# Kernel optimization log

Measured on AMD Instinct MI355X. Metric: run time of the kernel, lower is better.

Reference implementation:

```python
import jax, jax.numpy as jnp
import numpy as np

N_QUBITS = 4
N_LAYERS = 2
BN_EPS = 1e-5


def setup_inputs() -> dict:
    key = jax.random.key(0)
    k1, k2 = jax.random.split(key, 2)
    x = jax.random.normal(k1, (131072, 1, 28, 28), dtype=jnp.float32)
    q_params = jax.random.normal(k2, (N_LAYERS, N_QUBITS, 2), dtype=jnp.float32)
    gamma = jnp.ones((N_QUBITS,), dtype=jnp.float32)   # BatchNorm1d weight (init 1)
    beta = jnp.zeros((N_QUBITS,), dtype=jnp.float32)   # BatchNorm1d bias  (init 0)
    return {"x": x, "q_params": q_params, "gamma": gamma, "beta": beta}


def _apply_1q(state, U, w):
    """Apply 2x2 unitary U (shared across batch) on wire w. state: [B,2,2,2,2]."""
    s = jnp.moveaxis(state, 1 + w, -1)
    s = jnp.einsum('...j,ij->...i', s, U)
    return jnp.moveaxis(s, -1, 1 + w)


def _cnot(state, c, t):
    """CNOT with control c, target t on batched statevector [B,2,2,2,2]."""
    s = jnp.moveaxis(state, (1 + c, 1 + t), (-2, -1))
    s = jnp.stack([s[..., 0, :], s[..., 1, ::-1]], axis=-2)
    return jnp.moveaxis(s, (-2, -1), (1 + c, 1 + t))


def _circuit(enc, q_params):
    """Batched analytic statevector sim. enc: [B,4] RX angles -> [B,4] <Z_i>."""
    half = 0.5 * enc
    # RX(theta)|0> = [cos(t/2), -i sin(t/2)]; initial state is the outer product
    q = jnp.stack([jnp.cos(half).astype(jnp.complex64),
                   (-1j) * jnp.sin(half).astype(jnp.complex64)], axis=-1)  # [B,4,2]
    state = jnp.einsum('bi,bj,bk,bl->bijkl', q[:, 0], q[:, 1], q[:, 2], q[:, 3])
    for l in range(N_LAYERS):
        # RZ layer: pure diagonal phase, fuse all 4 wires into one [2,2,2,2] phase tensor
        a = 0.5 * q_params[l, :, 0]
        p = jnp.stack([jnp.exp(-1j * a), jnp.exp(1j * a)], axis=-1)  # [4,2]
        phase = jnp.einsum('i,j,k,l->ijkl', p[0], p[1], p[2], p[3])
        state = state * phase[None]
        # CNOT chain
        for c in range(N_QUBITS - 1):
            state = _cnot(state, c, c + 1)
        # RY layer
        b = 0.5 * q_params[l, :, 1]
        cb, sb = jnp.cos(b), jnp.sin(b)
        for w in range(N_QUBITS):
            U = jnp.stack([jnp.stack([cb[w], -sb[w]]),
                           jnp.stack([sb[w], cb[w]])]).astype(jnp.complex64)
            state = _apply_1q(state, U, w)
    probs = state.real ** 2 + state.imag ** 2  # [B,2,2,2,2]
    zs = []
    sign = jnp.array([1.0, -1.0], dtype=jnp.float32)
    for w in range(N_QUBITS):
        shp = [1] * 5
        shp[1 + w] = 2
        zs.append(jnp.sum(probs * sign.reshape(shp), axis=(1, 2, 3, 4)))
    return jnp.stack(zs, axis=1)  # [B,4]


def reference(x, q_params, gamma, beta):
    bsz = x.shape[0]
    # avg_pool2d(x, 6): kernel=stride=6, VALID -> [B,1,4,4]
    pooled = jax.lax.reduce_window(x, 0.0, jax.lax.add,
                                   (1, 1, 6, 6), (1, 1, 6, 6), 'VALID') / 36.0
    enc = pooled.reshape(bsz, -1)[:, :N_QUBITS]  # [B,4]
    out = _circuit(enc, q_params)                # [B,4]
    # BatchNorm1d in training mode: batch stats, biased variance
    mean = jnp.mean(out, axis=0)
    var = jnp.mean((out - mean) ** 2, axis=0)
    return (out - mean) / jnp.sqrt(var + BN_EPS) * gamma + beta
```

## Files before the change

### kernel.cpp

```cpp
#include <hip/hip_runtime.h>


__global__ __launch_bounds__(256) void qfc_main(
    const float* __restrict__ x,
    const float* __restrict__ qp,
    float* __restrict__ out,
    float* __restrict__ partials)
{
    const int tid  = threadIdx.x;
    const int gt   = blockIdx.x * 256 + tid;
    const int b    = gt >> 1;
    const int half = gt & 1;
    const float* px = x + (size_t)b * 784 + half * (3 * 28);

    float enc[4] = {0.f, 0.f, 0.f, 0.f};
    #pragma unroll
    for (int r = 0; r < 3; ++r) {
        const float4* row = (const float4*)(px + r * 28);
        #pragma unroll
        for (int q = 0; q < 6; ++q) {
            float4 v = row[q];
            const int c0 = q * 4;
            enc[(c0 + 0) / 6] += v.x;
            enc[(c0 + 1) / 6] += v.y;
            enc[(c0 + 2) / 6] += v.z;
            enc[(c0 + 3) / 6] += v.w;
        }
    }
    #pragma unroll
    for (int j = 0; j < 4; ++j)
        enc[j] += __shfl_xor(enc[j], 1, 64);

    float ch[4], sh[4];
    #pragma unroll
    for (int w = 0; w < 4; ++w) {
        float h = enc[w] * (0.5f / 36.0f);
        __sincosf(h, &sh[w], &ch[w]);
    }

    float sr[16], si[16];
    #pragma unroll
    for (int idx = 0; idx < 16; ++idx) {
        float m = 1.f; int k = 0;
        #pragma unroll
        for (int w = 0; w < 4; ++w) {
            if ((idx >> (3 - w)) & 1) { m *= sh[w]; ++k; }
            else                        m *= ch[w];
        }
        switch (k & 3) {
            case 0:  sr[idx] =  m;  si[idx] = 0.f; break;
            case 1:  sr[idx] = 0.f; si[idx] = -m;  break;
            case 2:  sr[idx] = -m;  si[idx] = 0.f; break;
            default: sr[idx] = 0.f; si[idx] =  m;  break;
        }
    }

    #pragma unroll
    for (int l = 0; l < 2; ++l) {
        #pragma unroll
        for (int w = 0; w < 4; ++w) {
            float a = 0.5f * qp[l * 8 + w * 2 + 0];
            float sa, ca; __sincosf(a, &sa, &ca);
            #pragma unroll
            for (int idx = 0; idx < 16; ++idx) {
                float sg = ((idx >> (3 - w)) & 1) ? sa : -sa;
                float r = sr[idx], mm = si[idx];
                sr[idx] = r * ca - mm * sg;
                si[idx] = r * sg + mm * ca;
            }
        }
        #pragma unroll
        for (int c = 0; c < 3; ++c) {
            const int t = c + 1;
            #pragma unroll
            for (int idx = 0; idx < 16; ++idx) {
                if ((((idx >> (3 - c)) & 1) == 1) && (((idx >> (3 - t)) & 1) == 0)) {
                    const int j = idx | (1 << (3 - t));
                    float tr = sr[idx]; sr[idx] = sr[j]; sr[j] = tr;
                    float ti = si[idx]; si[idx] = si[j]; si[j] = ti;
                }
            }
        }
        #pragma unroll
        for (int w = 0; w < 4; ++w) {
            float bb = 0.5f * qp[l * 8 + w * 2 + 1];
            float sb, cb; __sincosf(bb, &sb, &cb);
            #pragma unroll
            for (int idx = 0; idx < 16; ++idx) {
                if (((idx >> (3 - w)) & 1) == 0) {
                    const int j = idx | (1 << (3 - w));
                    float r0 = sr[idx], r1 = sr[j];
                    sr[idx] = cb * r0 - sb * r1;
                    sr[j]   = sb * r0 + cb * r1;
                    float i0 = si[idx], i1 = si[j];
                    si[idx] = cb * i0 - sb * i1;
                    si[j]   = sb * i0 + cb * i1;
                }
            }
        }
    }

    float o[4] = {0.f, 0.f, 0.f, 0.f};
    #pragma unroll
    for (int idx = 0; idx < 16; ++idx) {
        float p = sr[idx] * sr[idx] + si[idx] * si[idx];
        #pragma unroll
        for (int w = 0; w < 4; ++w)
            o[w] += ((idx >> (3 - w)) & 1) ? -p : p;
    }

    if (half == 0) {
        float4 ov; ov.x = o[0]; ov.y = o[1]; ov.z = o[2]; ov.w = o[3];
        ((float4*)out)[b] = ov;
    }

    const float g = (half == 0) ? 1.f : 0.f;
    float vals[8] = { g*o[0], g*o[1], g*o[2], g*o[3],
                      g*o[0]*o[0], g*o[1]*o[1], g*o[2]*o[2], g*o[3]*o[3] };
    #pragma unroll
    for (int q = 0; q < 8; ++q) {
        float v = vals[q];
        #pragma unroll
        for (int off = 32; off > 0; off >>= 1)
            v += __shfl_down(v, off, 64);
        vals[q] = v;
    }
    __shared__ float red[4][8];
    const int lane = tid & 63;
    const int wv   = tid >> 6;
    if (lane == 0) {
        #pragma unroll
        for (int q = 0; q < 8; ++q) red[wv][q] = vals[q];
    }
    __syncthreads();
    if (tid == 0) {
        #pragma unroll
        for (int q = 0; q < 8; ++q)
            partials[(size_t)blockIdx.x * 8 + q] =
                red[0][q] + red[1][q] + red[2][q] + red[3][q];
    }
}

__global__ __launch_bounds__(256) void qfc_stats_bn(
    const float* __restrict__ partials,
    const float* __restrict__ gamma,
    const float* __restrict__ beta,
    float* __restrict__ out,
    int nprt, int B)
{
    const int tid = threadIdx.x;
    double acc[8];
    #pragma unroll
    for (int q = 0; q < 8; ++q) acc[q] = 0.0;
    for (int r = tid; r < nprt; r += 256) {
        #pragma unroll
        for (int q = 0; q < 8; ++q) acc[q] += (double)partials[(size_t)r * 8 + q];
    }
    #pragma unroll
    for (int q = 0; q < 8; ++q) {
        double v = acc[q];
        #pragma unroll
        for (int off = 32; off > 0; off >>= 1)
            v += __shfl_down(v, off, 64);
        acc[q] = v;
    }
    __shared__ double dred[4][8];
    __shared__ float sstats[8];
    const int lane = tid & 63;
    const int wv   = tid >> 6;
    if (lane == 0) {
        #pragma unroll
        for (int q = 0; q < 8; ++q) dred[wv][q] = acc[q];
    }
    __syncthreads();
    if (tid == 0) {
        const double invB = 1.0 / (double)B;
        #pragma unroll
        for (int w = 0; w < 4; ++w) {
            double s  = dred[0][w]     + dred[1][w]     + dred[2][w]     + dred[3][w];
            double s2 = dred[0][4 + w] + dred[1][4 + w] + dred[2][4 + w] + dred[3][4 + w];
            double mean = s * invB;
            double var  = s2 * invB - mean * mean;
            double scl  = (double)gamma[w] / sqrt(var + 1e-5);
            sstats[w]     = (float)scl;
            sstats[4 + w] = (float)((double)beta[w] - mean * scl);
        }
    }
    __syncthreads();

    const int b = blockIdx.x * 256 + tid;
    float4 v = ((float4*)out)[b];
    v.x = v.x * sstats[0] + sstats[4];
    v.y = v.y * sstats[1] + sstats[5];
    v.z = v.z * sstats[2] + sstats[6];
    v.w = v.w * sstats[3] + sstats[7];
    ((float4*)out)[b] = v;
}

extern "C" void kernel_launch(void* const* d_in, const int* in_sizes, int n_in,
                              void* d_out, int out_size, void* d_ws, size_t ws_size,
                              hipStream_t stream)
{
    const float* x  = (const float*)d_in[0];
    const float* qp = (const float*)d_in[1];
    const float* gm = (const float*)d_in[2];
    const float* bt = (const float*)d_in[3];
    float* out = (float*)d_out;

    const int B     = in_sizes[0] / 784;
    const int nblk1 = (B * 2) / 256;
    const int nblk2 = B / 256;

    float* partials = (float*)d_ws;

    qfc_main    <<<nblk1, 256, 0, stream>>>(x, qp, out, partials);
    qfc_stats_bn<<<nblk2, 256, 0, stream>>>(partials, gm, bt, out, nblk1, B);
}
```

Measured before the change: 30.93 us.

## Stage pooling rows via async global-to-LDS loads with double buffering, one image per thread

The pooling phase now fetches the 6x24 pooled window of 64 images at a time into LDS with global_load_lds, double-buffering across four groups so the next group's loads overlap the current group's reduction. Four threads cooperate on each image's sum, and then each thread runs the full circuit for one image, which removes the duplicated half-thread circuit work and halves the grid. The cost is about 74KB of LDS per block and several barriers, which limits occupancy. Each block now also holds 256 images of serial load phases.

```diff
diff --git a/kernel.cpp b/kernel.cpp
--- a/kernel.cpp
+++ b/kernel.cpp
@@ -1,35 +1,89 @@
 #include <hip/hip_runtime.h>
 
 
-__global__ __launch_bounds__(256) void qfc_main(
+#define AS1 __attribute__((address_space(1)))
+#define AS3 __attribute__((address_space(3)))
+
+__device__ __forceinline__ void load_lds16(const float4* g, float4* l) {
+    __builtin_amdgcn_global_load_lds((const AS1 void*)g, (AS3 void*)l, 16, 0, 0);
+}
+
+__global__ __launch_bounds__(256, 2) void qfc_main(
     const float* __restrict__ x,
     const float* __restrict__ qp,
     float* __restrict__ out,
     float* __restrict__ partials)
 {
-    const int tid  = threadIdx.x;
-    const int gt   = blockIdx.x * 256 + tid;
-    const int b    = gt >> 1;
-    const int half = gt & 1;
-    const float* px = x + (size_t)b * 784 + half * (3 * 28);
-
-    float enc[4] = {0.f, 0.f, 0.f, 0.f};
-    #pragma unroll
-    for (int r = 0; r < 3; ++r) {
-        const float4* row = (const float4*)(px + r * 28);
-        #pragma unroll
-        for (int q = 0; q < 6; ++q) {
-            float4 v = row[q];
+    __shared__ float4 stage[2][2304];
+    __shared__ float4 encs[256];
+    __shared__ float  red[4][8];
+
+    const int tid   = threadIdx.x;
+    const int wid   = tid >> 6;
+    const int lane  = tid & 63;
+    const int gimg0 = blockIdx.x * 256;
+    const float4* x4 = (const float4*)x;
+
+    #pragma unroll
+    for (int k = 0; k < 9; ++k) {
+        const int sb  = k * 256 + wid * 64;
+        const int p   = sb + lane;
+        const int im  = p / 36;
+        const int rq  = p - im * 36;
+        const int r   = rq / 6;
+        const int q   = rq - r * 6;
+        load_lds16(x4 + (size_t)(gimg0 + im) * 196 + r * 7 + q, &stage[0][sb]);
+    }
+    __syncthreads();
+
+    const int img = tid >> 2;
+    const int sub = tid & 3;
+
+    #pragma unroll
+    for (int g = 0; g < 4; ++g) {
+        const int cur = g & 1;
+        if (g < 3) {
+            const int nxt = cur ^ 1;
+            #pragma unroll
+            for (int k = 0; k < 9; ++k) {
+                const int sb = k * 256 + wid * 64;
+                const int p  = sb + lane;
+                const int im = p / 36;
+                const int rq = p - im * 36;
+                const int r  = rq / 6;
+                const int q  = rq - r * 6;
+                load_lds16(x4 + (size_t)(gimg0 + (g + 1) * 64 + im) * 196 + r * 7 + q,
+                           &stage[nxt][sb]);
+            }
+        }
+        float enc0 = 0.f, enc1 = 0.f, enc2 = 0.f, enc3 = 0.f;
+        #pragma unroll
+        for (int i = 0; i < 9; ++i) {
+            const int rq = sub * 9 + i;
+            const int r  = rq / 6;
+            const int q  = rq - r * 6;
+            const float4 v = stage[cur][img * 36 + rq];
             const int c0 = q * 4;
-            enc[(c0 + 0) / 6] += v.x;
-            enc[(c0 + 1) / 6] += v.y;
-            enc[(c0 + 2) / 6] += v.z;
-            enc[(c0 + 3) / 6] += v.w;
-        }
-    }
-    #pragma unroll
-    for (int j = 0; j < 4; ++j)
-        enc[j] += __shfl_xor(enc[j], 1, 64);
+            const int j0 = (c0 + 0) / 6, j1 = (c0 + 1) / 6;
+            const int j2 = (c0 + 2) / 6, j3 = (c0 + 3) / 6;
+            enc0 += (j0 == 0 ? v.x : 0.f) + (j1 == 0 ? v.y : 0.f) + (j2 == 0 ? v.z : 0.f) + (j3 == 0 ? v.w : 0.f);
+            enc1 += (j0 == 1 ? v.x : 0.f) + (j1 == 1 ? v.y : 0.f) + (j2 == 1 ? v.z : 0.f) + (j3 == 1 ? v.w : 0.f);
+            enc2 += (j0 == 2 ? v.x : 0.f) + (j1 == 2 ? v.y : 0.f) + (j2 == 2 ? v.z : 0.f) + (j3 == 2 ? v.w : 0.f);
+            enc3 += (j0 == 3 ? v.x : 0.f) + (j1 == 3 ? v.y : 0.f) + (j2 == 3 ? v.z : 0.f) + (j3 == 3 ? v.w : 0.f);
+        }
+        enc0 += __shfl_xor(enc0, 1, 64); enc1 += __shfl_xor(enc1, 1, 64);
+        enc2 += __shfl_xor(enc2, 1, 64); enc3 += __shfl_xor(enc3, 1, 64);
+        enc0 += __shfl_xor(enc0, 2, 64); enc1 += __shfl_xor(enc1, 2, 64);
+        enc2 += __shfl_xor(enc2, 2, 64); enc3 += __shfl_xor(enc3, 2, 64);
+        if (sub == 0) {
+            float4 e; e.x = enc0; e.y = enc1; e.z = enc2; e.w = enc3;
+            encs[g * 64 + img] = e;
+        }
+        __syncthreads();
+    }
+
+    const float4 e = encs[tid];
+    float enc[4] = { e.x, e.y, e.z, e.w };
 
     float ch[4], sh[4];
     #pragma unroll
@@ -109,14 +163,12 @@
             o[w] += ((idx >> (3 - w)) & 1) ? -p : p;
     }
 
-    if (half == 0) {
-        float4 ov; ov.x = o[0]; ov.y = o[1]; ov.z = o[2]; ov.w = o[3];
-        ((float4*)out)[b] = ov;
-    }
-
-    const float g = (half == 0) ? 1.f : 0.f;
-    float vals[8] = { g*o[0], g*o[1], g*o[2], g*o[3],
-                      g*o[0]*o[0], g*o[1]*o[1], g*o[2]*o[2], g*o[3]*o[3] };
+    const int b = gimg0 + tid;
+    float4 ov; ov.x = o[0]; ov.y = o[1]; ov.z = o[2]; ov.w = o[3];
+    ((float4*)out)[b] = ov;
+
+    float vals[8] = { o[0], o[1], o[2], o[3],
+                      o[0]*o[0], o[1]*o[1], o[2]*o[2], o[3]*o[3] };
     #pragma unroll
     for (int q = 0; q < 8; ++q) {
         float v = vals[q];
@@ -125,12 +177,9 @@
             v += __shfl_down(v, off, 64);
         vals[q] = v;
     }
-    __shared__ float red[4][8];
-    const int lane = tid & 63;
-    const int wv   = tid >> 6;
     if (lane == 0) {
         #pragma unroll
-        for (int q = 0; q < 8; ++q) red[wv][q] = vals[q];
+        for (int q = 0; q < 8; ++q) red[wid][q] = vals[q];
     }
     __syncthreads();
     if (tid == 0) {
@@ -207,12 +256,11 @@
     const float* bt = (const float*)d_in[3];
     float* out = (float*)d_out;
 
-    const int B     = in_sizes[0] / 784;
-    const int nblk1 = (B * 2) / 256;
-    const int nblk2 = B / 256;
+    const int B    = in_sizes[0] / 784;
+    const int nblk = B / 256;
 
     float* partials = (float*)d_ws;
 
-    qfc_main    <<<nblk1, 256, 0, stream>>>(x, qp, out, partials);
-    qfc_stats_bn<<<nblk2, 256, 0, stream>>>(partials, gm, bt, out, nblk1, B);
-}
+    qfc_main    <<<nblk, 256, 0, stream>>>(x, qp, out, partials);
+    qfc_stats_bn<<<nblk, 256, 0, stream>>>(partials, gm, bt, out, nblk, B);
+}
```

Result: slower. 32.59 us (+5.4%).
